# Kernel tuning notes

Hardware: AMD Instinct MI355X
Metric: run time of the kernel (lower is better)

The kernel has to match this reference:

```python
import jax, jax.numpy as jnp
import numpy as np

C, B, N, L = 4, 8, 4096, 1024


def setup_inputs() -> dict:
    key = jax.random.key(0)
    inputs = jax.random.normal(key, (C, B, N, L), dtype=jnp.float32)
    return {"inputs": inputs}


def reference(inputs) -> jnp.ndarray:
    # Original: for each [N, L] box_input, divide each row elementwise by
    # range(1..L) and reduce_sum over the last axis. Vectorized across all
    # leading dims via broadcasting. Output shape [C, B, N].
    L_ = inputs.shape[-1]
    probability_numbers = jnp.arange(1, L_ + 1, dtype=inputs.dtype)  # [L]
    return jnp.sum(inputs / probability_numbers, axis=-1)
```

## Files before the change

kernel.cpp:

```cpp
#include <hip/hip_runtime.h>


constexpr int kL = 1024;

__global__ __launch_bounds__(256) void FractalDimension_kernel(
    const float* __restrict__ in, float* __restrict__ out) {
  const int row = blockIdx.x;
  const int tid = threadIdx.x;

  const float4* p = reinterpret_cast<const float4*>(in + (size_t)row * kL);
  float4 v = p[tid];

  const float b0 = (float)(4 * tid + 1);
  float s = v.x / b0 + v.y / (b0 + 1.0f) + v.z / (b0 + 2.0f) + v.w / (b0 + 3.0f);

  #pragma unroll
  for (int off = 32; off > 0; off >>= 1)
    s += __shfl_down(s, off, 64);

  __shared__ float partial[4];
  const int wave = tid >> 6;
  if ((tid & 63) == 0) partial[wave] = s;
  __syncthreads();

  if (tid == 0)
    out[row] = (partial[0] + partial[1]) + (partial[2] + partial[3]);
}

extern "C" void kernel_launch(void* const* d_in, const int* in_sizes, int n_in,
                              void* d_out, int out_size, void* d_ws, size_t ws_size,
                              hipStream_t stream) {
  const float* in = (const float*)d_in[0];
  float* out = (float*)d_out;
  const int rows = in_sizes[0] / kL;
  FractalDimension_kernel<<<rows, 256, 0, stream>>>(in, out);
}
```

Baseline: 648.3 us.

## Use persistent wave-per-row kernel with precomputed reciprocal weights

Result: slower. 667.2 us (+2.9%).

```diff
diff --git a/kernel.cpp b/kernel.cpp
--- a/kernel.cpp
+++ b/kernel.cpp
@@ -2,29 +2,57 @@
 
 
 constexpr int kL = 1024;
+constexpr int kBlocks = 2048;
+constexpr int kThreads = 256;
 
-__global__ __launch_bounds__(256) void FractalDimension_kernel(
-    const float* __restrict__ in, float* __restrict__ out) {
-  const int row = blockIdx.x;
-  const int tid = threadIdx.x;
+__global__ __launch_bounds__(kThreads) void FractalDimension_kernel(
+    const float* __restrict__ in, float* __restrict__ out, int rows) {
+  const int lane = threadIdx.x & 63;
+  const int waveId = blockIdx.x * (kThreads >> 6) + (threadIdx.x >> 6);
+  const int nWaves = kBlocks * (kThreads >> 6);
 
-  const float4* p = reinterpret_cast<const float4*>(in + (size_t)row * kL);
-  float4 v = p[tid];
+  float r[4][4];
+#pragma unroll
+  for (int k = 0; k < 4; ++k)
+#pragma unroll
+    for (int c = 0; c < 4; ++c)
+      r[k][c] = 1.0f / (float)((lane + k * 64) * 4 + c + 1);
 
-  const float b0 = (float)(4 * tid + 1);
-  float s = v.x / b0 + v.y / (b0 + 1.0f) + v.z / (b0 + 2.0f) + v.w / (b0 + 3.0f);
+  const int trips = rows / nWaves;
+#pragma unroll 2
+  for (int i = 0; i < trips; ++i) {
+    const int row = waveId + i * nWaves;
+    const float4* p = reinterpret_cast<const float4*>(in + (size_t)row * kL);
+    float4 v0 = p[lane];
+    float4 v1 = p[lane + 64];
+    float4 v2 = p[lane + 128];
+    float4 v3 = p[lane + 192];
 
-  #pragma unroll
-  for (int off = 32; off > 0; off >>= 1)
-    s += __shfl_down(s, off, 64);
+    float s = v0.x * r[0][0] + v0.y * r[0][1] + v0.z * r[0][2] + v0.w * r[0][3];
+    s += v1.x * r[1][0] + v1.y * r[1][1] + v1.z * r[1][2] + v1.w * r[1][3];
+    s += v2.x * r[2][0] + v2.y * r[2][1] + v2.z * r[2][2] + v2.w * r[2][3];
+    s += v3.x * r[3][0] + v3.y * r[3][1] + v3.z * r[3][2] + v3.w * r[3][3];
 
-  __shared__ float partial[4];
-  const int wave = tid >> 6;
-  if ((tid & 63) == 0) partial[wave] = s;
-  __syncthreads();
+#pragma unroll
+    for (int off = 32; off > 0; off >>= 1)
+      s += __shfl_down(s, off, 64);
 
-  if (tid == 0)
-    out[row] = (partial[0] + partial[1]) + (partial[2] + partial[3]);
+    if (lane == 0) out[row] = s;
+  }
+
+  for (int row = trips * nWaves + waveId; row < rows; row += nWaves) {
+    const float4* p = reinterpret_cast<const float4*>(in + (size_t)row * kL);
+    float s = 0.f;
+#pragma unroll
+    for (int k = 0; k < 4; ++k) {
+      float4 v = p[lane + k * 64];
+      s += v.x * r[k][0] + v.y * r[k][1] + v.z * r[k][2] + v.w * r[k][3];
+    }
+#pragma unroll
+    for (int off = 32; off > 0; off >>= 1)
+      s += __shfl_down(s, off, 64);
+    if (lane == 0) out[row] = s;
+  }
 }
 
 extern "C" void kernel_launch(void* const* d_in, const int* in_sizes, int n_in,
@@ -33,5 +61,5 @@
   const float* in = (const float*)d_in[0];
   float* out = (float*)d_out;
   const int rows = in_sizes[0] / kL;
-  FractalDimension_kernel<<<rows, 256, 0, stream>>>(in, out);
+  FractalDimension_kernel<<<kBlocks, kThreads, 0, stream>>>(in, out, rows);
 }
```
